# Kernel tuning notes

Hardware: AMD Instinct MI355X
Metric: run time of the kernel (lower is better)

## Reference

```python
import jax, jax.numpy as jnp
import numpy as np

B, L, H, F, E = 32, 512, 768, 3072, 8  # sentences, seq_len, hidden, ffn, experts


def setup_inputs() -> dict:
    key = jax.random.key(0)
    kx, kl, k1, k2, k3, k4 = jax.random.split(key, 6)
    return {
        "hidden_states": jax.random.normal(kx, (B, L, H), dtype=jnp.float32),
        "router_labels": jax.random.randint(kl, (B,), 0, E, dtype=jnp.int32),
        "W1": jax.random.normal(k1, (E, H, F), dtype=jnp.float32) * 0.02,
        "b1": jnp.zeros((E, F), dtype=jnp.float32),
        "W2": jax.random.normal(k2, (E, F, H), dtype=jnp.float32) * 0.02,
        "b2": jnp.zeros((E, H), dtype=jnp.float32),
    }


def reference(hidden_states, router_labels, W1, b1, W2, b2):
    # Equivalent to: sort sentences by label, run each group through its
    # expert FFN, concat, unsort. Expressed as a gather of per-sentence
    # expert weights followed by batched GEMMs (same math, no data-dependent
    # shapes).
    W1g = W1[router_labels]            # [B, H, F]
    b1g = b1[router_labels][:, None]   # [B, 1, F]
    W2g = W2[router_labels]            # [B, F, H]
    b2g = b2[router_labels][:, None]   # [B, 1, H]
    h = jnp.einsum("blh,bhf->blf", hidden_states, W1g) + b1g
    h = jax.nn.gelu(h, approximate=False)
    out = jnp.einsum("blf,bfh->blh", h, W2g) + b2g
    return out
```

## Files before the change

### kernel.cpp

```cpp
#include <hip/hip_runtime.h>
#include <hip/hip_bf16.h>

#define NB   32
#define SEQ  512
#define HID  768
#define FFN  3072
#define NEXP 8

typedef float f32x4 __attribute__((ext_vector_type(4)));
typedef short s16x8 __attribute__((ext_vector_type(8)));

__device__ __forceinline__ unsigned short f2bf(float f) {
    return __builtin_bit_cast(unsigned short, (__bf16)f);
}

__device__ __forceinline__ float fast_exp2(float x) {
    float r; asm("v_exp_f32 %0, %1" : "=v"(r) : "v"(x)); return r;
}
__device__ __forceinline__ float fast_rcp(float x) {
    float r; asm("v_rcp_f32 %0, %1" : "=v"(r) : "v"(x)); return r;
}

__device__ __forceinline__ float gelu_fast(float v) {
    float u  = v * (0.7978845608f + 0.0356774081f * v * v);
    float t  = fast_exp2(-2.8853900817779268f * fabsf(u));
    float T  = (1.0f - t) * fast_rcp(1.0f + t);
    return 0.5f * v + 0.5f * fabsf(v) * T;
}

#define GLOAD16(gp, lp) __builtin_amdgcn_global_load_lds( \
    (const __attribute__((address_space(1))) unsigned int*)(gp), \
    (__attribute__((address_space(3))) unsigned int*)(lp), 16, 0, 0)

__global__ void sort_labels_kernel(const int* __restrict__ labels, int* __restrict__ perm)
{
    int i = threadIdx.x;
    if (i < NB) {
        int li = labels[i];
        int rank = 0;
        for (int j = 0; j < NB; j++) {
            int lj = labels[j];
            if (lj < li || (lj == li && j < i)) rank++;
        }
        perm[rank] = i;
    }
}

__global__ __launch_bounds__(256) void cvt_x_kernel(
    const float* __restrict__ X, unsigned short* __restrict__ Xb, int n8)
{
    int idx = blockIdx.x * blockDim.x + threadIdx.x;
    int stride = gridDim.x * blockDim.x;
    for (int i = idx; i < n8; i += stride) {
        f32x4 a = *(const f32x4*)(X + (size_t)i * 8);
        f32x4 b = *(const f32x4*)(X + (size_t)i * 8 + 4);
        unsigned short o[8];
#pragma unroll
        for (int v = 0; v < 4; v++) o[v] = f2bf(a[v]);
#pragma unroll
        for (int v = 0; v < 4; v++) o[4 + v] = f2bf(b[v]);
        *(s16x8*)(Xb + (size_t)i * 8) = *(s16x8*)o;
    }
}

__global__ __launch_bounds__(256) void cvt_transpose_kernel(
    const float* __restrict__ W, unsigned short* __restrict__ WT, int R, int C)
{
    __shared__ unsigned short tile[64][65];
    const int cb = blockIdx.x * 64, rb = blockIdx.y * 64;
    const float* src = W + (size_t)blockIdx.z * R * C;
    unsigned short* dst = WT + (size_t)blockIdx.z * R * C;
    const int x = threadIdx.x & 63, y0 = threadIdx.x >> 6;
#pragma unroll
    for (int i = 0; i < 16; i++) {
        int r = y0 + i * 4;
        tile[r][x] = f2bf(src[(size_t)(rb + r) * C + cb + x]);
    }
    __syncthreads();
#pragma unroll
    for (int i = 0; i < 16; i++) {
        int c = y0 + i * 4;
        dst[(size_t)(cb + c) * R + rb + x] = tile[x][c];
    }
}

template<int LDB, bool ISA>
__device__ __forceinline__ void stage_region(const char* g, char* lds, int half, int tid)
{
#pragma unroll
    for (int p = 0; p < 2; p++) {
        int L  = p * 8192 + tid * 16;
        int rr = L >> 7;
        int cb = L & 127;
        int row = ISA ? ((rr & 63) + ((rr >> 6) << 7) + half * 64)
                      : ((rr & 31) + ((rr >> 5) << 6) + half * 32);
        int cbs = cb ^ ((row & 7) << 4);
        GLOAD16(g + (size_t)row * LDB + cbs, lds + (size_t)row * 128 + cb);
    }
}

__device__ __forceinline__ void read_af(const char* Ab, int arow_b, int k0, int ih, s16x8 (&a)[2][4])
{
    const int k1 = k0 ^ 64;
#pragma unroll
    for (int i = 0; i < 4; i++) {
        const char* p = Ab + arow_b + (ih * 64 + i * 16) * 128;
        a[0][i] = *(const s16x8*)(p + k0);
        a[1][i] = *(const s16x8*)(p + k1);
    }
}
__device__ __forceinline__ void read_bf(const char* Bb, int brow_b, int k0, int jh, s16x8 (&b)[2][2])
{
    const int k1 = k0 ^ 64;
#pragma unroll
    for (int j = 0; j < 2; j++) {
        const char* p = Bb + brow_b + (jh * 32 + j * 16) * 128;
        b[0][j] = *(const s16x8*)(p + k0);
        b[1][j] = *(const s16x8*)(p + k1);
    }
}

template<int IH, int JH>
__device__ __forceinline__ void mfma_quad(s16x8 (&a)[2][4], s16x8 (&b)[2][2], f32x4 (&acc)[8][4])
{
    __builtin_amdgcn_s_setprio(1);
#pragma unroll
    for (int kk = 0; kk < 2; kk++)
#pragma unroll
        for (int i = 0; i < 4; i++)
#pragma unroll
            for (int j = 0; j < 2; j++)
                acc[IH * 4 + i][JH * 2 + j] = __builtin_amdgcn_mfma_f32_16x16x32_bf16(
                    a[kk][i], b[kk][j], acc[IH * 4 + i][JH * 2 + j], 0, 0, 0);
    __builtin_amdgcn_s_setprio(0);
}

template<int LDB, bool S1, bool S2, int VM>
__device__ __forceinline__ void gwindow(const char* AgK, const char* BgK,
    char* Acur, char* Bcur, char* Anxt, char* Bnxt,
    int arow_b, int brow_b, int k0, int tid, f32x4 (&acc)[8][4])
{
    s16x8 a[2][4], b0[2][2], b1[2][2];
    read_af(Acur, arow_b, k0, 0, a);
    read_bf(Bcur, brow_b, k0, 0, b0);
    if constexpr (S1) stage_region<LDB, true >(AgK + 128, Anxt, 1, tid);
    __builtin_amdgcn_s_barrier();
    mfma_quad<0, 0>(a, b0, acc);
    __builtin_amdgcn_s_barrier();
    read_bf(Bcur, brow_b, k0, 1, b1);
    if constexpr (S1) stage_region<LDB, false>(BgK + 128, Bnxt, 1, tid);
    __builtin_amdgcn_s_barrier();
    mfma_quad<0, 1>(a, b1, acc);
    __builtin_amdgcn_s_barrier();
    read_af(Acur, arow_b, k0, 1, a);
    if constexpr (S2) stage_region<LDB, true >(AgK + 256, Acur, 0, tid);
    __builtin_amdgcn_s_barrier();
    mfma_quad<1, 1>(a, b1, acc);
    __builtin_amdgcn_s_barrier();
    if constexpr (S2) stage_region<LDB, false>(BgK + 256, Bcur, 0, tid);
    __builtin_amdgcn_s_barrier();
    mfma_quad<1, 0>(a, b0, acc);
    if constexpr (VM >= 0)
        asm volatile("s_waitcnt vmcnt(%0)" :: "i"(VM) : "memory");
    __builtin_amdgcn_s_barrier();
}

template<int LDB>
__device__ __forceinline__ void gemm_mainloop(const char* Ag, const char* Bg,
    char* smem, int KT, int tid, int arow_b, int brow_b, int k0, f32x4 (&acc)[8][4])
{
    stage_region<LDB, true >(Ag,       smem,          0, tid);
    stage_region<LDB, false>(Bg,       smem + 65536,  0, tid);
    stage_region<LDB, true >(Ag,       smem,          1, tid);
    stage_region<LDB, false>(Bg,       smem + 65536,  1, tid);
    stage_region<LDB, true >(Ag + 128, smem + 32768,  0, tid);
    stage_region<LDB, false>(Bg + 128, smem + 98304,  0, tid);
    asm volatile("s_waitcnt vmcnt(4)" ::: "memory");
    __builtin_amdgcn_s_barrier();

    int cur = 0;
    for (int kt = 0; kt < KT - 2; ++kt) {
        char* Acur = smem + (cur << 15);
        char* Anxt = smem + ((cur ^ 1) << 15);
        char* Bcur = smem + 65536 + (cur << 15);
        char* Bnxt = smem + 65536 + ((cur ^ 1) << 15);
        gwindow<LDB, true, true, 4>(Ag + (size_t)kt * 128, Bg + (size_t)kt * 128,
            Acur, Bcur, Anxt, Bnxt, arow_b, brow_b, k0, tid, acc);
        cur ^= 1;
    }
    {
        char* Acur = smem + (cur << 15);
        char* Anxt = smem + ((cur ^ 1) << 15);
        char* Bcur = smem + 65536 + (cur << 15);
        char* Bnxt = smem + 65536 + ((cur ^ 1) << 15);
        gwindow<LDB, true, false, 0>(Ag + (size_t)(KT - 2) * 128, Bg + (size_t)(KT - 2) * 128,
            Acur, Bcur, Anxt, Bnxt, arow_b, brow_b, k0, tid, acc);
        cur ^= 1;
    }
    {
        char* Acur = smem + (cur << 15);
        char* Anxt = smem + ((cur ^ 1) << 15);
        char* Bcur = smem + 65536 + (cur << 15);
        char* Bnxt = smem + 65536 + ((cur ^ 1) << 15);
        gwindow<LDB, false, false, -1>(Ag + (size_t)(KT - 1) * 128, Bg + (size_t)(KT - 1) * 128,
            Acur, Bcur, Anxt, Bnxt, arow_b, brow_b, k0, tid, acc);
    }
}

__global__ __launch_bounds__(512, 2) void moe_gemm1(
    const unsigned short* __restrict__ Xb,
    const int*   __restrict__ labels,
    const int*   __restrict__ perm,
    const unsigned short* __restrict__ W1T,
    const float* __restrict__ B1,
    unsigned short* __restrict__ G)
{
    extern __shared__ char smem[];
    const int L = blockIdx.x;
    const int xcd = L & 7, s = L >> 3;
    const int bs = perm[xcd * 4 + s / 24];
    const int rr = s % 24;
    const int mt = rr / 12, nt = rr % 12;
    const int e  = labels[bs];

    const char* Ag = (const char*)(Xb + ((size_t)bs * SEQ + (size_t)mt * 256) * HID);
    const char* Bg = (const char*)(W1T + (size_t)e * FFN * HID + (size_t)nt * 256 * HID);

    const int tid = threadIdx.x;
    const int lane = tid & 63, w = tid >> 6;
    const int wm = (w >> 2) * 128, wn = (w & 3) * 64;
    const int fr = lane & 15, fq = lane >> 4;
    const int arow_b = (wm + fr) * 128, brow_b = (wn + fr) * 128;
    const int k0 = (fq * 16) ^ ((fr & 7) << 4);

    f32x4 acc[8][4];
#pragma unroll
    for (int i = 0; i < 8; i++)
#pragma unroll
        for (int j = 0; j < 4; j++) acc[i][j] = (f32x4)0.0f;

    gemm_mainloop<HID * 2>(Ag, Bg, smem, HID / 64, tid, arow_b, brow_b, k0, acc);

    const float* b1g = B1 + (size_t)e * FFN + (size_t)nt * 256;
    unsigned short* Cg = G + ((size_t)bs * SEQ + (size_t)mt * 256) * FFN + (size_t)nt * 256;
    float bias[4];
#pragma unroll
    for (int nj = 0; nj < 4; nj++) bias[nj] = b1g[wn + nj * 16 + fr];
#pragma unroll
    for (int mi = 0; mi < 8; mi++)
#pragma unroll
        for (int nj = 0; nj < 4; nj++) {
            const int col = wn + nj * 16 + fr;
#pragma unroll
            for (int r = 0; r < 4; r++) {
                const int row = wm + mi * 16 + fq * 4 + r;
                float v = acc[mi][nj][r] + bias[nj];
                Cg[(size_t)row * FFN + col] = f2bf(gelu_fast(v));
            }
        }
}

__global__ __launch_bounds__(512, 2) void moe_gemm2(
    const unsigned short* __restrict__ G,
    const int*   __restrict__ labels,
    const int*   __restrict__ perm,
    const unsigned short* __restrict__ W2T,
    const float* __restrict__ B2,
    float* __restrict__ Out)
{
    extern __shared__ char smem[];
    const int L = blockIdx.x;
    const int xcd = L & 7, s = L >> 3;
    const int bs = perm[xcd * 4 + s / 6];
    const int rr = s % 6;
    const int mt = rr / 3, nt = rr % 3;
    const int e  = labels[bs];

    const char* Ag = (const char*)(G + ((size_t)bs * SEQ + (size_t)mt * 256) * FFN);
    const char* Bg = (const char*)(W2T + (size_t)e * HID * FFN + (size_t)nt * 256 * FFN);

    const int tid = threadIdx.x;
    const int lane = tid & 63, w = tid >> 6;
    const int wm = (w >> 2) * 128, wn = (w & 3) * 64;
    const int fr = lane & 15, fq = lane >> 4;
    const int arow_b = (wm + fr) * 128, brow_b = (wn + fr) * 128;
    const int k0 = (fq * 16) ^ ((fr & 7) << 4);

    f32x4 acc[8][4];
#pragma unroll
    for (int i = 0; i < 8; i++)
#pragma unroll
        for (int j = 0; j < 4; j++) acc[i][j] = (f32x4)0.0f;

    gemm_mainloop<FFN * 2>(Ag, Bg, smem, FFN / 64, tid, arow_b, brow_b, k0, acc);

    const float* b2g = B2 + (size_t)e * HID + (size_t)nt * 256;
    float* Cg = Out + ((size_t)bs * SEQ + (size_t)mt * 256) * HID + (size_t)nt * 256;
    float bias[4];
#pragma unroll
    for (int nj = 0; nj < 4; nj++) bias[nj] = b2g[wn + nj * 16 + fr];
#pragma unroll
    for (int mi = 0; mi < 8; mi++)
#pragma unroll
        for (int nj = 0; nj < 4; nj++) {
            const int col = wn + nj * 16 + fr;
#pragma unroll
            for (int r = 0; r < 4; r++) {
                const int row = wm + mi * 16 + fq * 4 + r;
                Cg[(size_t)row * HID + col] = acc[mi][nj][r] + bias[nj];
            }
        }
}

extern "C" void kernel_launch(void* const* d_in, const int* in_sizes, int n_in,
                              void* d_out, int out_size, void* d_ws, size_t ws_size,
                              hipStream_t stream) {
    const float* X      = (const float*)d_in[0];
    const int*   labels = (const int*)  d_in[1];
    const float* W1     = (const float*)d_in[2];
    const float* B1     = (const float*)d_in[3];
    const float* W2     = (const float*)d_in[4];
    const float* B2     = (const float*)d_in[5];
    float* Out = (float*)d_out;

    char* ws = (char*)d_ws;
    unsigned short* Xb  = (unsigned short*)(ws);
    unsigned short* W1T = (unsigned short*)(ws + 25165824);
    unsigned short* W2T = (unsigned short*)(ws + 62914560);
    unsigned short* G   = (unsigned short*)(ws + 100663296);
    int*            perm = (int*)(ws + 201326592);

    (void)hipFuncSetAttribute((const void*)moe_gemm1,
        hipFuncAttributeMaxDynamicSharedMemorySize, 131072);
    (void)hipFuncSetAttribute((const void*)moe_gemm2,
        hipFuncAttributeMaxDynamicSharedMemorySize, 131072);

    sort_labels_kernel<<<1, 64, 0, stream>>>(labels, perm);
    cvt_x_kernel<<<2048, 256, 0, stream>>>(X, Xb, NB * SEQ * HID / 8);
    cvt_transpose_kernel<<<dim3(FFN / 64, HID / 64, NEXP), 256, 0, stream>>>(W1, W1T, HID, FFN);
    cvt_transpose_kernel<<<dim3(HID / 64, FFN / 64, NEXP), 256, 0, stream>>>(W2, W2T, FFN, HID);

    moe_gemm1<<<768, dim3(512), 131072, stream>>>(Xb, labels, perm, W1T, B1, G);
    moe_gemm2<<<192, dim3(512), 131072, stream>>>(G, labels, perm, W2T, B2, Out);
}
```

Before: 236.8 us.

## Rewrite GEMM1 with dedicated producer wave and 4-slot LDS ring

Replaces the first expert GEMM with a warp-specialised kernel. One extra wave issues all global-to-LDS loads into a 4-slot ring buffer, while eight compute waves run MFMA on a smaller 256x128 tile with K-steps of 32. The tile is halved, so the grid doubles to 1536 blocks and LDS per block drops to 96KB, with launch bounds aiming for 3 blocks per CU. The aim is to overlap loads with compute and raise occupancy. The cost is less data reuse per tile and a barrier on every K-step.

```diff
diff --git a/kernel.cpp b/kernel.cpp
--- a/kernel.cpp
+++ b/kernel.cpp
@@ -31,6 +31,8 @@
 #define GLOAD16(gp, lp) __builtin_amdgcn_global_load_lds( \
     (const __attribute__((address_space(1))) unsigned int*)(gp), \
     (__attribute__((address_space(3))) unsigned int*)(lp), 16, 0, 0)
+
+#define VMCNT(N) asm volatile("s_waitcnt vmcnt(%0)" :: "i"(N) : "memory")
 
 __global__ void sort_labels_kernel(const int* __restrict__ labels, int* __restrict__ perm)
 {
@@ -84,6 +86,150 @@
     }
 }
 
+__global__ __launch_bounds__(576, 3) void moe_gemm1(
+    const unsigned short* __restrict__ Xb,
+    const int*   __restrict__ labels,
+    const int*   __restrict__ perm,
+    const unsigned short* __restrict__ W1T,
+    const float* __restrict__ B1,
+    unsigned short* __restrict__ G)
+{
+    extern __shared__ char smem[];
+    const int L = blockIdx.x;
+    const int xcd = L & 7, s = L >> 3;
+    const int bs = perm[xcd * 4 + s / 48];
+    const int rr = s % 48;
+    const int mt = rr / 24, nt = rr % 24;
+    const int e  = labels[bs];
+
+    const char* Ag = (const char*)(Xb + ((size_t)bs * SEQ + (size_t)mt * 256) * HID);
+    const char* Bg = (const char*)(W1T + (size_t)e * FFN * HID + (size_t)nt * 128 * HID);
+
+    const int tid  = threadIdx.x;
+    const int wid  = tid >> 6, lane = tid & 63;
+    const int KT   = HID / 32;
+
+    if (wid == 8) {
+        const int r4  = lane >> 2;
+        const int ch  = (lane & 3) * 16;
+        for (int k = 0; k < KT; ++k) {
+            if (k == 0) {
+#pragma unroll
+                for (int w = 0; w < 2; w++) {
+                    char* slot = smem + (w & 3) * 24576;
+                    const char* ga = Ag + w * 64;
+                    const char* gb = Bg + w * 64;
+#pragma unroll
+                    for (int i = 0; i < 16; i++) {
+                        int row = i * 16 + r4;
+                        int src = ch ^ (((row >> 1) & 3) << 4);
+                        GLOAD16(ga + (size_t)row * (HID * 2) + src, slot + i * 1024 + lane * 16);
+                    }
+#pragma unroll
+                    for (int i = 0; i < 8; i++) {
+                        int row = i * 16 + r4;
+                        int src = ch ^ (((row >> 1) & 3) << 4);
+                        GLOAD16(gb + (size_t)row * (HID * 2) + src, slot + 16384 + i * 1024 + lane * 16);
+                    }
+                }
+            }
+            if (k + 2 < KT) {
+                int w = k + 2;
+                char* slot = smem + (w & 3) * 24576;
+                const char* ga = Ag + w * 64;
+                const char* gb = Bg + w * 64;
+#pragma unroll
+                for (int i = 0; i < 16; i++) {
+                    int row = i * 16 + r4;
+                    int src = ch ^ (((row >> 1) & 3) << 4);
+                    GLOAD16(ga + (size_t)row * (HID * 2) + src, slot + i * 1024 + lane * 16);
+                }
+#pragma unroll
+                for (int i = 0; i < 8; i++) {
+                    int row = i * 16 + r4;
+                    int src = ch ^ (((row >> 1) & 3) << 4);
+                    GLOAD16(gb + (size_t)row * (HID * 2) + src, slot + 16384 + i * 1024 + lane * 16);
+                }
+                VMCNT(48);
+            } else if (k + 1 < KT) {
+                VMCNT(24);
+            } else {
+                VMCNT(0);
+            }
+            __builtin_amdgcn_s_barrier();
+        }
+        return;
+    }
+
+    const int fr = lane & 15, fq = lane >> 4;
+    const int wm = (wid >> 1) * 64, wn = (wid & 1) * 64;
+
+    int aoff[4], boff[4];
+#pragma unroll
+    for (int i = 0; i < 4; i++) {
+        int arow = wm + i * 16 + fr;
+        aoff[i] = arow * 64 + ((fq * 16) ^ (((arow >> 1) & 3) << 4));
+        int brow = wn + i * 16 + fr;
+        boff[i] = 16384 + brow * 64 + ((fq * 16) ^ (((brow >> 1) & 3) << 4));
+    }
+
+    f32x4 acc[4][4];
+#pragma unroll
+    for (int i = 0; i < 4; i++)
+#pragma unroll
+        for (int j = 0; j < 4; j++) acc[i][j] = (f32x4)0.0f;
+
+    for (int k = 0; k < KT; ++k) {
+        if (k > 0) {
+            const char* slot = smem + ((k - 1) & 3) * 24576;
+            s16x8 av[4], bv[4];
+#pragma unroll
+            for (int i = 0; i < 4; i++) av[i] = *(const s16x8*)(slot + aoff[i]);
+#pragma unroll
+            for (int j = 0; j < 4; j++) bv[j] = *(const s16x8*)(slot + boff[j]);
+            __builtin_amdgcn_s_setprio(1);
+#pragma unroll
+            for (int i = 0; i < 4; i++)
+#pragma unroll
+                for (int j = 0; j < 4; j++)
+                    acc[i][j] = __builtin_amdgcn_mfma_f32_16x16x32_bf16(av[i], bv[j], acc[i][j], 0, 0, 0);
+            __builtin_amdgcn_s_setprio(0);
+        }
+        __syncthreads();
+    }
+    {
+        const char* slot = smem + ((KT - 1) & 3) * 24576;
+        s16x8 av[4], bv[4];
+#pragma unroll
+        for (int i = 0; i < 4; i++) av[i] = *(const s16x8*)(slot + aoff[i]);
+#pragma unroll
+        for (int j = 0; j < 4; j++) bv[j] = *(const s16x8*)(slot + boff[j]);
+#pragma unroll
+        for (int i = 0; i < 4; i++)
+#pragma unroll
+            for (int j = 0; j < 4; j++)
+                acc[i][j] = __builtin_amdgcn_mfma_f32_16x16x32_bf16(av[i], bv[j], acc[i][j], 0, 0, 0);
+    }
+
+    const float* b1g = B1 + (size_t)e * FFN + (size_t)nt * 128;
+    unsigned short* Cg = G + ((size_t)bs * SEQ + (size_t)mt * 256) * FFN + (size_t)nt * 128;
+    float bias[4];
+#pragma unroll
+    for (int nj = 0; nj < 4; nj++) bias[nj] = b1g[wn + nj * 16 + fr];
+#pragma unroll
+    for (int mi = 0; mi < 4; mi++)
+#pragma unroll
+        for (int nj = 0; nj < 4; nj++) {
+            const int col = wn + nj * 16 + fr;
+#pragma unroll
+            for (int r2 = 0; r2 < 4; r2++) {
+                const int row = wm + mi * 16 + fq * 4 + r2;
+                float v = acc[mi][nj][r2] + bias[nj];
+                Cg[(size_t)row * FFN + col] = f2bf(gelu_fast(v));
+            }
+        }
+}
+
 template<int LDB, bool ISA>
 __device__ __forceinline__ void stage_region(const char* g, char* lds, int half, int tid)
 {
@@ -160,8 +306,7 @@
     if constexpr (S2) stage_region<LDB, false>(BgK + 256, Bcur, 0, tid);
     __builtin_amdgcn_s_barrier();
     mfma_quad<1, 0>(a, b0, acc);
-    if constexpr (VM >= 0)
-        asm volatile("s_waitcnt vmcnt(%0)" :: "i"(VM) : "memory");
+    if constexpr (VM >= 0) VMCNT(VM);
     __builtin_amdgcn_s_barrier();
 }
 
@@ -175,7 +320,7 @@
     stage_region<LDB, false>(Bg,       smem + 65536,  1, tid);
     stage_region<LDB, true >(Ag + 128, smem + 32768,  0, tid);
     stage_region<LDB, false>(Bg + 128, smem + 98304,  0, tid);
-    asm volatile("s_waitcnt vmcnt(4)" ::: "memory");
+    VMCNT(4);
     __builtin_amdgcn_s_barrier();
 
     int cur = 0;
@@ -205,59 +350,6 @@
         gwindow<LDB, false, false, -1>(Ag + (size_t)(KT - 1) * 128, Bg + (size_t)(KT - 1) * 128,
             Acur, Bcur, Anxt, Bnxt, arow_b, brow_b, k0, tid, acc);
     }
-}
-
-__global__ __launch_bounds__(512, 2) void moe_gemm1(
-    const unsigned short* __restrict__ Xb,
-    const int*   __restrict__ labels,
-    const int*   __restrict__ perm,
-    const unsigned short* __restrict__ W1T,
-    const float* __restrict__ B1,
-    unsigned short* __restrict__ G)
-{
-    extern __shared__ char smem[];
-    const int L = blockIdx.x;
-    const int xcd = L & 7, s = L >> 3;
-    const int bs = perm[xcd * 4 + s / 24];
-    const int rr = s % 24;
-    const int mt = rr / 12, nt = rr % 12;
-    const int e  = labels[bs];
-
-    const char* Ag = (const char*)(Xb + ((size_t)bs * SEQ + (size_t)mt * 256) * HID);
-    const char* Bg = (const char*)(W1T + (size_t)e * FFN * HID + (size_t)nt * 256 * HID);
-
-    const int tid = threadIdx.x;
-    const int lane = tid & 63, w = tid >> 6;
-    const int wm = (w >> 2) * 128, wn = (w & 3) * 64;
-    const int fr = lane & 15, fq = lane >> 4;
-    const int arow_b = (wm + fr) * 128, brow_b = (wn + fr) * 128;
-    const int k0 = (fq * 16) ^ ((fr & 7) << 4);
-
-    f32x4 acc[8][4];
-#pragma unroll
-    for (int i = 0; i < 8; i++)
-#pragma unroll
-        for (int j = 0; j < 4; j++) acc[i][j] = (f32x4)0.0f;
-
-    gemm_mainloop<HID * 2>(Ag, Bg, smem, HID / 64, tid, arow_b, brow_b, k0, acc);
-
-    const float* b1g = B1 + (size_t)e * FFN + (size_t)nt * 256;
-    unsigned short* Cg = G + ((size_t)bs * SEQ + (size_t)mt * 256) * FFN + (size_t)nt * 256;
-    float bias[4];
-#pragma unroll
-    for (int nj = 0; nj < 4; nj++) bias[nj] = b1g[wn + nj * 16 + fr];
-#pragma unroll
-    for (int mi = 0; mi < 8; mi++)
-#pragma unroll
-        for (int nj = 0; nj < 4; nj++) {
-            const int col = wn + nj * 16 + fr;
-#pragma unroll
-            for (int r = 0; r < 4; r++) {
-                const int row = wm + mi * 16 + fq * 4 + r;
-                float v = acc[mi][nj][r] + bias[nj];
-                Cg[(size_t)row * FFN + col] = f2bf(gelu_fast(v));
-            }
-        }
 }
 
 __global__ __launch_bounds__(512, 2) void moe_gemm2(
@@ -331,7 +423,7 @@
     int*            perm = (int*)(ws + 201326592);
 
     (void)hipFuncSetAttribute((const void*)moe_gemm1,
-        hipFuncAttributeMaxDynamicSharedMemorySize, 131072);
+        hipFuncAttributeMaxDynamicSharedMemorySize, 98304);
     (void)hipFuncSetAttribute((const void*)moe_gemm2,
         hipFuncAttributeMaxDynamicSharedMemorySize, 131072);
 
@@ -340,6 +432,6 @@
     cvt_transpose_kernel<<<dim3(FFN / 64, HID / 64, NEXP), 256, 0, stream>>>(W1, W1T, HID, FFN);
     cvt_transpose_kernel<<<dim3(HID / 64, FFN / 64, NEXP), 256, 0, stream>>>(W2, W2T, FFN, HID);
 
-    moe_gemm1<<<768, dim3(512), 131072, stream>>>(Xb, labels, perm, W1T, B1, G);
-    moe_gemm2<<<192, dim3(512), 131072, stream>>>(G, labels, perm, W2T, B2, Out);
-}
+    moe_gemm1<<<1536, dim3(576), 98304, stream>>>(Xb, labels, perm, W1T, B1, G);
+    moe_gemm2<<<192,  dim3(512), 131072, stream>>>(G, labels, perm, W2T, B2, Out);
+}
```

After: 259.3 us. +9.5%, slower.
